# Kernel tuning notes

Hardware: AMD Instinct MI355X
Metric: run time of the kernel (lower is better)

## Reference

```python
import jax, jax.numpy as jnp
import numpy as np

VOCAB, D, BLOCK = 32000, 1024, 2048
B, S = 4, 2048

def setup_inputs() -> dict:
    key = jax.random.key(0)
    ks = jax.random.split(key, 12)
    s = 0.02
    return {
        "x": jax.random.randint(ks[0], (B, S), 0, VOCAB),
        "tok_emb": jax.random.normal(ks[1], (VOCAB, D), jnp.float32) * s,
        "pos_emb": jax.random.normal(ks[2], (BLOCK, D), jnp.float32) * s,
        "Wq": jax.random.normal(ks[3], (D, D), jnp.float32) * s,
        "bq": jnp.zeros((D,), jnp.float32),
        "Wk": jax.random.normal(ks[4], (D, D), jnp.float32) * s,
        "bk": jnp.zeros((D,), jnp.float32),
        "Wv": jax.random.normal(ks[5], (D, D), jnp.float32) * s,
        "bv": jnp.zeros((D,), jnp.float32),
        "Wfc": jax.random.normal(ks[6], (VOCAB, D), jnp.float32) * s,
        "bfc": jnp.zeros((VOCAB,), jnp.float32),
    }

def reference(x, tok_emb, pos_emb, Wq, bq, Wk, bk, Wv, bv, Wfc, bfc):
    # embeddings: token lookup + learned positional
    h = tok_emb[x] + pos_emb[jnp.arange(x.shape[1])][None, :, :]  # [B,S,D]
    Q = h @ Wq.T + bq
    K = h @ Wk.T + bk
    V = h @ Wv.T + bv
    scale = 1.0 / jnp.sqrt(jnp.float32(Q.shape[-1]))
    scores = jnp.einsum('bqd,bkd->bqk', Q, K) * scale  # [B,S,S]
    attn = jax.nn.softmax(scores, axis=-1)
    out = jnp.einsum('bqk,bkd->bqd', attn, V)
    return out @ Wfc.T + bfc  # [B,S,VOCAB]
```

## Files before the change

### kernel.cpp

```cpp
#include <hip/hip_runtime.h>
#include <hip/hip_bf16.h>
#include <stdint.h>

typedef __bf16 bf16x8 __attribute__((ext_vector_type(8)));
typedef float f32x4 __attribute__((ext_vector_type(4)));
typedef unsigned short u16x8 __attribute__((ext_vector_type(8)));

#define DEVINL static __device__ __forceinline__

DEVINL unsigned short f2bf(float f) {
  unsigned u = __builtin_bit_cast(unsigned, f);
  unsigned r = (u + 0x7FFFu + ((u >> 16) & 1u)) >> 16;
  return (unsigned short)r;
}
DEVINL float bf2f(unsigned short u) {
  return __builtin_bit_cast(float, ((unsigned)u) << 16);
}

DEVINL void gload_lds16(const unsigned short* g, unsigned short* l) {
  __builtin_amdgcn_global_load_lds(
      (const __attribute__((address_space(1))) void*)g,
      (__attribute__((address_space(3))) void*)l, 16, 0, 0);
}

__global__ __launch_bounds__(256) void embed_cvtq_kernel(
    const int* __restrict__ x, const float* __restrict__ tok,
    const float* __restrict__ pos, unsigned short* __restrict__ hb,
    const float* __restrict__ wq, const float* __restrict__ wk,
    const float* __restrict__ wv, unsigned short* __restrict__ wqkvb)
{
  if (blockIdx.x >= 8192) {
    const int b = blockIdx.x - 8192;
    for (long i = (long)b * 256 + threadIdx.x; i < 786432; i += 512 * 256) {
      const float* src;
      long off;
      if (i < 262144)      { src = wq; off = i; }
      else if (i < 524288) { src = wk; off = i - 262144; }
      else                 { src = wv; off = i - 524288; }
      float4 v = ((const float4*)src)[off];
      ushort4 o;
      o.x = f2bf(v.x); o.y = f2bf(v.y); o.z = f2bf(v.z); o.w = f2bf(v.w);
      ((ushort4*)wqkvb)[i] = o;
    }
    return;
  }
  const int bs = blockIdx.x;
  const int s  = bs & 2047;
  const long trow = (long)x[bs] * 1024;
  const int d = threadIdx.x * 4;
  const float4 t = *(const float4*)(tok + trow + d);
  const float4 p = *(const float4*)(pos + (long)s * 1024 + d);
  ushort4 o;
  o.x = f2bf(t.x + p.x);
  o.y = f2bf(t.y + p.y);
  o.z = f2bf(t.z + p.z);
  o.w = f2bf(t.w + p.w);
  *(ushort4*)(hb + (long)bs * 1024 + d) = o;
}

template<int OUTMODE>
__global__ __launch_bounds__(256) void gemm_bt(
    const unsigned short* __restrict__ A, const unsigned short* __restrict__ B,
    void* __restrict__ Cout, const float* __restrict__ bias,
    float scale, int M, int N, int K,
    long sA, long sB, long sC, int Mb, long tStride, int mapMode)
{
  __shared__ __align__(16) unsigned short lA[128 * 32];
  __shared__ __align__(16) unsigned short lB[128 * 32];
  const int tid = threadIdx.x, wid = tid >> 6, lane = tid & 63;
  int bx, by, bz;
  if (mapMode == 0) {
    bx = blockIdx.x; by = blockIdx.y; bz = blockIdx.z;
  } else {
    const int bid = blockIdx.x;
    const int g = bid & 7, jj = bid >> 3;
    bz = g >> 1;
    by = (g & 1) * 8 + (jj & 7);
    bx = jj >> 3;
  }
  A += (long)bz * sA;
  B += (long)bz * sB;
  const int bm = by * 128, bn = bx * 128;

  const int c0 = wid * 64 + lane, c1 = c0 + 256;
  const unsigned short* gA0 = A + (long)(bm + (c0 >> 2)) * K + (c0 & 3) * 8;
  const unsigned short* gA1 = A + (long)(bm + (c1 >> 2)) * K + (c1 & 3) * 8;
  const unsigned short* gB0 = B + (long)(bn + (c0 >> 2)) * K + (c0 & 3) * 8;
  const unsigned short* gB1 = B + (long)(bn + (c1 >> 2)) * K + (c1 & 3) * 8;
  unsigned short* lA0 = lA + wid * 512;
  unsigned short* lA1 = lA + 2048 + wid * 512;
  unsigned short* lB0 = lB + wid * 512;
  unsigned short* lB1 = lB + 2048 + wid * 512;

  const int wr = (wid >> 1) * 64, wc = (wid & 1) * 64;
  const int lr = lane & 15, lk = (lane >> 4) * 8;

  f32x4 acc[4][4] = {};
  const int nk = K >> 5;
  for (int kt = 0; kt < nk; ++kt) {
    const int ko = kt << 5;
    gload_lds16(gA0 + ko, lA0);
    gload_lds16(gA1 + ko, lA1);
    gload_lds16(gB0 + ko, lB0);
    gload_lds16(gB1 + ko, lB1);
    __syncthreads();
    bf16x8 af[4], bg[4];
#pragma unroll
    for (int m = 0; m < 4; ++m)
      af[m] = *(const bf16x8*)(const void*)(lA + (wr + m * 16 + lr) * 32 + lk);
#pragma unroll
    for (int n = 0; n < 4; ++n)
      bg[n] = *(const bf16x8*)(const void*)(lB + (wc + n * 16 + lr) * 32 + lk);
#pragma unroll
    for (int m = 0; m < 4; ++m)
#pragma unroll
      for (int n = 0; n < 4; ++n)
        acc[m][n] = __builtin_amdgcn_mfma_f32_16x16x32_bf16(af[m], bg[n],
                                                            acc[m][n], 0, 0, 0);
    __syncthreads();
  }

  const int r0 = bm + wr + ((lane >> 4) << 2);
  const int cbase = bn + wc + lr;
#pragma unroll
  for (int n = 0; n < 4; ++n) {
    const int col = cbase + n * 16;
    const float bv = bias ? bias[col] : 0.f;
#pragma unroll
    for (int m = 0; m < 4; ++m) {
      const int row0 = r0 + m * 16;
      if (OUTMODE == 2) {
        float* C = (float*)Cout + (long)bz * sC;
#pragma unroll
        for (int i = 0; i < 4; ++i)
          C[(long)(row0 + i) * N + col] = acc[m][n][i] * scale + bv;
      } else if (OUTMODE == 0) {
        unsigned short* C = (unsigned short*)Cout + (long)bz * sC;
#pragma unroll
        for (int i = 0; i < 4; ++i)
          C[(long)(row0 + i) * N + col] = f2bf(acc[m][n][i] * scale + bv);
      } else {
        unsigned short* C = (unsigned short*)Cout;
        const int b = row0 / Mb;
        const int srow = row0 - b * Mb;
        ushort4 o;
        o.x = f2bf(acc[m][n][0] * scale + bv);
        o.y = f2bf(acc[m][n][1] * scale + bv);
        o.z = f2bf(acc[m][n][2] * scale + bv);
        o.w = f2bf(acc[m][n][3] * scale + bv);
        *(ushort4*)(C + (long)b * tStride + (long)col * Mb + srow) = o;
      }
    }
  }
}

__global__ __launch_bounds__(256) void scores_cvt_kernel(
    const unsigned short* __restrict__ Qb, const unsigned short* __restrict__ Kb,
    unsigned short* __restrict__ Sc,
    const float* __restrict__ wfc, unsigned short* __restrict__ wfcb)
{
  __shared__ __align__(16) unsigned short lA[128 * 32];
  __shared__ __align__(16) unsigned short lB[128 * 32];
  if (blockIdx.x < 1024) {
    for (long i = (long)blockIdx.x * 256 + threadIdx.x; i < 8192000;
         i += 1024 * 256) {
      float4 v = ((const float4*)wfc)[i];
      ushort4 o;
      o.x = f2bf(v.x); o.y = f2bf(v.y); o.z = f2bf(v.z); o.w = f2bf(v.w);
      ((ushort4*)wfcb)[i] = o;
    }
    return;
  }
  constexpr int K = 1024, N = 2048;
  const int tid = threadIdx.x, wid = tid >> 6, lane = tid & 63;
  const int bid = blockIdx.x - 1024;
  const int g = bid & 7, jj = bid >> 3;
  const int bz = g >> 1;
  const int by = (g & 1) * 8 + (jj & 7);
  const int bx = jj >> 3;
  const unsigned short* A = Qb + (long)bz * (2048L * 1024);
  const unsigned short* B = Kb + (long)bz * (2048L * 1024);
  unsigned short* C = Sc + (long)bz * (2048L * 2048);
  const int bm = by * 128, bn = bx * 128;

  const int c0 = wid * 64 + lane, c1 = c0 + 256;
  const unsigned short* gA0 = A + (long)(bm + (c0 >> 2)) * K + (c0 & 3) * 8;
  const unsigned short* gA1 = A + (long)(bm + (c1 >> 2)) * K + (c1 & 3) * 8;
  const unsigned short* gB0 = B + (long)(bn + (c0 >> 2)) * K + (c0 & 3) * 8;
  const unsigned short* gB1 = B + (long)(bn + (c1 >> 2)) * K + (c1 & 3) * 8;
  unsigned short* lA0 = lA + wid * 512;
  unsigned short* lA1 = lA + 2048 + wid * 512;
  unsigned short* lB0 = lB + wid * 512;
  unsigned short* lB1 = lB + 2048 + wid * 512;

  const int wr = (wid >> 1) * 64, wc = (wid & 1) * 64;
  const int lr = lane & 15, lk = (lane >> 4) * 8;

  f32x4 acc[4][4] = {};
  for (int kt = 0; kt < 32; ++kt) {
    const int ko = kt << 5;
    gload_lds16(gA0 + ko, lA0);
    gload_lds16(gA1 + ko, lA1);
    gload_lds16(gB0 + ko, lB0);
    gload_lds16(gB1 + ko, lB1);
    __syncthreads();
    bf16x8 af[4], bg[4];
#pragma unroll
    for (int m = 0; m < 4; ++m)
      af[m] = *(const bf16x8*)(const void*)(lA + (wr + m * 16 + lr) * 32 + lk);
#pragma unroll
    for (int n = 0; n < 4; ++n)
      bg[n] = *(const bf16x8*)(const void*)(lB + (wc + n * 16 + lr) * 32 + lk);
#pragma unroll
    for (int m = 0; m < 4; ++m)
#pragma unroll
      for (int n = 0; n < 4; ++n)
        acc[m][n] = __builtin_amdgcn_mfma_f32_16x16x32_bf16(af[m], bg[n],
                                                            acc[m][n], 0, 0, 0);
    __syncthreads();
  }

  const int r0 = bm + wr + ((lane >> 4) << 2);
  const int cbase = bn + wc + lr;
#pragma unroll
  for (int n = 0; n < 4; ++n) {
    const int col = cbase + n * 16;
#pragma unroll
    for (int m = 0; m < 4; ++m) {
      const int row0 = r0 + m * 16;
#pragma unroll
      for (int i = 0; i < 4; ++i)
        C[(long)(row0 + i) * N + col] = f2bf(acc[m][n][i] * 0.03125f);
    }
  }
}

__global__ __launch_bounds__(256) void softmax_kernel(unsigned short* __restrict__ S)
{
  unsigned short* row = S + (long)blockIdx.x * 2048;
  const int t = threadIdx.x, lane = t & 63, wid = t >> 6;
  __shared__ float redm[4], reds[4];
  u16x8 raw = ((const u16x8*)row)[t];
  float v[8];
#pragma unroll
  for (int j = 0; j < 8; ++j) v[j] = bf2f(raw[j]);
  float mx = v[0];
#pragma unroll
  for (int j = 1; j < 8; ++j) mx = fmaxf(mx, v[j]);
#pragma unroll
  for (int off = 32; off; off >>= 1) mx = fmaxf(mx, __shfl_xor(mx, off, 64));
  if (lane == 0) redm[wid] = mx;
  __syncthreads();
  mx = fmaxf(fmaxf(redm[0], redm[1]), fmaxf(redm[2], redm[3]));
  float s = 0.f;
#pragma unroll
  for (int j = 0; j < 8; ++j) { v[j] = __expf(v[j] - mx); s += v[j]; }
#pragma unroll
  for (int off = 32; off; off >>= 1) s += __shfl_xor(s, off, 64);
  if (lane == 0) reds[wid] = s;
  __syncthreads();
  s = reds[0] + reds[1] + reds[2] + reds[3];
  const float inv = 1.f / s;
  u16x8 o;
#pragma unroll
  for (int j = 0; j < 8; ++j) o[j] = f2bf(v[j] * inv);
  ((u16x8*)row)[t] = o;
}

DEVINL bf16x8 ldfrag(const unsigned short* p, int row, int kx) {
  return *(const bf16x8*)((const char*)p + row * 128 + kx);
}

#define BARSB() do { __builtin_amdgcn_s_barrier(); \
                     __builtin_amdgcn_sched_barrier(0); } while (0)
#define LGK0() asm volatile("s_waitcnt lgkmcnt(0)")
#define VM6()  asm volatile("s_waitcnt vmcnt(6)")

#define MF16(rb, aArr, bArr) do { \
  _Pragma("unroll") for (int m_ = 0; m_ < 4; ++m_) \
  _Pragma("unroll") for (int n_ = 0; n_ < 4; ++n_) \
    acc[(rb) + m_][n_] = __builtin_amdgcn_mfma_f32_16x16x32_bf16( \
        aArr[m_], bArr[n_], acc[(rb) + m_][n_], 0, 0, 0); \
} while (0)

#define STG_A(b, h, gk) do { \
  const char* s_ = srcA + (h) * 262144 + (long)(((gk) & 15)) * 128; \
  gload_lds16((const unsigned short*)(s_ + la0), \
              dA + (b) * 16384 + (h) * 8192 + dO0); \
  gload_lds16((const unsigned short*)(s_ + la1), \
              dA + (b) * 16384 + (h) * 8192 + dO1); } while (0)
#define STG_B(b, h, gk) do { \
  int t_ = (gk) >> 4; if (t_ >= len) t_ = len - 1; \
  const char* s_ = Bbase + ((long)(bnStart + t_) << 19) + \
                   (h) * 262144 + (long)(((gk) & 15)) * 128; \
  gload_lds16((const unsigned short*)(s_ + la0), \
              dB + (b) * 16384 + (h) * 8192 + dO0); \
  gload_lds16((const unsigned short*)(s_ + la1), \
              dB + (b) * 16384 + (h) * 8192 + dO1); } while (0)

#define KTILE(BUF, S1, S2, S3, S4) do { \
  bf16x8 b0_[4], b1_[4], aA_[4], aB_[4], aC_[4], aD_[4]; \
  _Pragma("unroll") for (int n = 0; n < 4; ++n) { \
    b0_[n] = ldfrag(dB + (BUF) * 16384, wn * 64 + n * 16 + lr, kx0); \
    b1_[n] = ldfrag(dB + (BUF) * 16384, wn * 64 + n * 16 + lr, kx1); } \
  _Pragma("unroll") for (int m = 0; m < 4; ++m) \
    aA_[m] = ldfrag(dA + (BUF) * 16384, wm * 128 + m * 16 + lr, kx0); \
  S1; \
  BARSB(); LGK0(); __builtin_amdgcn_s_setprio(1); \
  MF16(0, aA_, b0_); \
  __builtin_amdgcn_s_setprio(0); BARSB(); \
  _Pragma("unroll") for (int m = 0; m < 4; ++m) { \
    aB_[m] = ldfrag(dA + (BUF) * 16384, wm * 128 + (4 + m) * 16 + lr, kx0); \
    aC_[m] = ldfrag(dA + (BUF) * 16384, wm * 128 + (4 + m) * 16 + lr, kx1); } \
  S2; \
  BARSB(); LGK0(); __builtin_amdgcn_s_setprio(1); \
  MF16(4, aB_, b0_); \
  __builtin_amdgcn_s_setprio(0); BARSB(); \
  _Pragma("unroll") for (int m = 0; m < 4; ++m) \
    aD_[m] = ldfrag(dA + (BUF) * 16384, wm * 128 + m * 16 + lr, kx1); \
  S3; \
  BARSB(); LGK0(); __builtin_amdgcn_s_setprio(1); \
  MF16(4, aC_, b1_); \
  __builtin_amdgcn_s_setprio(0); BARSB(); \
  S4; VM6(); \
  BARSB(); LGK0(); __builtin_amdgcn_s_setprio(1); \
  MF16(0, aD_, b1_); \
  __builtin_amdgcn_s_setprio(0); BARSB(); \
} while (0)

#define G256_PRELUDE() \
  const int tid = threadIdx.x, wid = tid >> 6, lane = tid & 63; \
  const int wm = wid >> 2, wn = wid & 3; \
  const int lr = lane & 15; \
  const int kq = (lane >> 4) << 4; \
  const int xr = (lane & 7) << 4; \
  const int kx0 = kq ^ xr; \
  const int kx1 = (64 | kq) ^ xr; \
  const int loff0 = wid * 1024 + lane * 16; \
  const int loff1 = loff0 + 8192; \
  const int r0 = loff0 >> 7, r1 = loff1 >> 7; \
  const int c0 = (loff0 & 127) ^ ((r0 & 7) << 4); \
  const int c1 = (loff1 & 127) ^ ((r1 & 7) << 4); \
  const long la0 = (long)r0 * 2048 + c0; \
  const long la1 = (long)r1 * 2048 + c1; \
  unsigned short* dA = lds; \
  unsigned short* dB = lds + 32768; \
  const int dO0 = wid * 512, dO1 = 4096 + wid * 512

__global__ __launch_bounds__(512, 2) void gemm256_fc(
    const unsigned short* __restrict__ A, const unsigned short* __restrict__ B,
    float* __restrict__ C, const float* __restrict__ bias)
{
  constexpr int N = 32000;
  __shared__ __align__(16) unsigned short lds[65536];
  G256_PRELUDE();

  const int bid = blockIdx.x;
  const int g = bid & 7;
  const int j = bid >> 3;
  const int bm = g * 4 + (j & 3);
  const int q = j >> 2;
  const int bnStart = (q < 5) ? 16 * q : 80 + (q - 5) * 15;
  const int len = (q < 5) ? 16 : 15;

  const char* srcA = (const char*)A + ((long)bm << 19);
  const char* Bbase = (const char*)B;

  f32x4 acc[8][4] = {};
  float bv[4];
#pragma unroll
  for (int n = 0; n < 4; ++n)
    bv[n] = bias[(long)bnStart * 256 + wn * 64 + n * 16 + lr];

  STG_B(0, 0, 0); STG_B(0, 1, 0); STG_A(0, 0, 0); STG_A(0, 1, 0);
  STG_B(1, 0, 1); STG_B(1, 1, 1); STG_A(1, 0, 1);
  VM6();
  BARSB();

  for (int t = 0; t < len; ++t) {
#pragma unroll 1
    for (int it = 0; it < 8; ++it) {
      const int gk = t * 16 + 2 * it;
      KTILE(0, STG_A(1, 1, gk + 1), STG_B(0, 0, gk + 2), STG_B(0, 1, gk + 2),
            STG_A(0, 0, gk + 2));
      KTILE(1, STG_A(0, 1, gk + 2), STG_B(1, 0, gk + 3), STG_B(1, 1, gk + 3),
            STG_A(1, 0, gk + 3));
    }
    const long bnRow = ((long)bnStart + t) * 256;
    const int q4 = (lane >> 4) * 4;
#pragma unroll
    for (int m = 0; m < 8; ++m) {
      const long row = (long)bm * 256 + wm * 128 + m * 16 + q4;
#pragma unroll
      for (int i = 0; i < 4; ++i) {
        float* orow = C + (row + i) * (long)N;
#pragma unroll
        for (int n = 0; n < 4; ++n)
          __builtin_nontemporal_store(acc[m][n][i] + bv[n],
                                      &orow[bnRow + wn * 64 + n * 16 + lr]);
      }
    }
    VM6();
    const int tn = (t + 1 < len) ? t + 1 : t;
#pragma unroll
    for (int n = 0; n < 4; ++n)
      bv[n] = bias[((long)bnStart + tn) * 256 + wn * 64 + n * 16 + lr];
#pragma unroll
    for (int m = 0; m < 8; ++m)
#pragma unroll
      for (int n = 0; n < 4; ++n)
        acc[m][n] = f32x4{0.f, 0.f, 0.f, 0.f};
  }
}

__global__ __launch_bounds__(512, 2) void gemm256_qkv(
    const unsigned short* __restrict__ A, const unsigned short* __restrict__ B,
    unsigned short* __restrict__ Qb, unsigned short* __restrict__ Kb,
    unsigned short* __restrict__ Vt,
    const float* __restrict__ bq, const float* __restrict__ bk,
    const float* __restrict__ bv)
{
  __shared__ __align__(16) unsigned short lds[65536];
  G256_PRELUDE();

  const int bid = blockIdx.x;
  const int g = bid & 7;
  const int j = bid >> 3;
  const int bm = g * 4 + (j & 3);
  const int q = j >> 2;
  const int bnStart = (q < 4) ? 2 * q : 8 + (q - 4);
  const int len = (q < 4) ? 2 : 1;

  const char* srcA = (const char*)A + ((long)bm << 19);
  const char* Bbase = (const char*)B;

  f32x4 acc[8][4] = {};

  STG_B(0, 0, 0); STG_B(0, 1, 0); STG_A(0, 0, 0); STG_A(0, 1, 0);
  STG_B(1, 0, 1); STG_B(1, 1, 1); STG_A(1, 0, 1);
  VM6();
  BARSB();

  for (int t = 0; t < len; ++t) {
#pragma unroll 1
    for (int it = 0; it < 8; ++it) {
      const int gk = t * 16 + 2 * it;
      KTILE(0, STG_A(1, 1, gk + 1), STG_B(0, 0, gk + 2), STG_B(0, 1, gk + 2),
            STG_A(0, 0, gk + 2));
      KTILE(1, STG_A(0, 1, gk + 2), STG_B(1, 0, gk + 3), STG_B(1, 1, gk + 3),
            STG_A(1, 0, gk + 3));
    }
    const int bnT = bnStart + t;
    const int sector = bnT >> 2;
    const int colb = (bnT & 3) * 256;
    const float* bias_s = (sector == 0) ? bq : (sector == 1) ? bk : bv;
    const int q4 = (lane >> 4) * 4;
    if (sector < 2) {
      unsigned short* C = (sector == 0) ? Qb : Kb;
#pragma unroll
      for (int n = 0; n < 4; ++n) {
        const int col = colb + wn * 64 + n * 16 + lr;
        const float bb = bias_s[col];
#pragma unroll
        for (int m = 0; m < 8; ++m) {
          const long row = (long)bm * 256 + wm * 128 + m * 16 + q4;
#pragma unroll
          for (int i = 0; i < 4; ++i)
            C[(row + i) * 1024 + col] = f2bf(acc[m][n][i] + bb);
        }
      }
    } else {
#pragma unroll
      for (int n = 0; n < 4; ++n) {
        const int col = colb + wn * 64 + n * 16 + lr;
        const float bb = bias_s[col];
#pragma unroll
        for (int m = 0; m < 8; ++m) {
          const long row = (long)bm * 256 + wm * 128 + m * 16 + q4;
          const int b = (int)(row >> 11);
          const int srow = (int)(row & 2047);
          ushort4 o;
          o.x = f2bf(acc[m][n][0] + bb);
          o.y = f2bf(acc[m][n][1] + bb);
          o.z = f2bf(acc[m][n][2] + bb);
          o.w = f2bf(acc[m][n][3] + bb);
          *(ushort4*)(Vt + (long)b * (1024L * 2048) + (long)col * 2048 + srow) = o;
        }
      }
    }
    VM6();
#pragma unroll
    for (int m = 0; m < 8; ++m)
#pragma unroll
      for (int n = 0; n < 4; ++n)
        acc[m][n] = f32x4{0.f, 0.f, 0.f, 0.f};
  }
}

extern "C" void kernel_launch(void* const* d_in, const int* in_sizes, int n_in,
                              void* d_out, int out_size, void* d_ws, size_t ws_size,
                              hipStream_t stream)
{
  const int*   x   = (const int*)d_in[0];
  const float* tok = (const float*)d_in[1];
  const float* pos = (const float*)d_in[2];
  const float* Wq  = (const float*)d_in[3];
  const float* bq  = (const float*)d_in[4];
  const float* Wk  = (const float*)d_in[5];
  const float* bk  = (const float*)d_in[6];
  const float* Wv  = (const float*)d_in[7];
  const float* bv  = (const float*)d_in[8];
  const float* Wfc = (const float*)d_in[9];
  const float* bfc = (const float*)d_in[10];
  float* out = (float*)d_out;

  char* ws = (char*)d_ws;
  unsigned short* hb   = (unsigned short*)(ws);
  unsigned short* Wqb  = (unsigned short*)(ws + 16777216);
  unsigned short* Wfcb = (unsigned short*)(ws + 23068672);
  unsigned short* Qb   = (unsigned short*)(ws + 88604672);
  unsigned short* Kb   = (unsigned short*)(ws + 105381888);
  unsigned short* Vt   = (unsigned short*)(ws + 122159104);
  unsigned short* Sc   = (unsigned short*)(ws + 138936320);
  unsigned short* AO   = hb;

  dim3 blk(256);
  embed_cvtq_kernel<<<dim3(8704), blk, 0, stream>>>(x, tok, pos, hb,
                                                    Wq, Wk, Wv, Wqb);
  gemm256_qkv<<<dim3(256), dim3(512), 0, stream>>>(hb, Wqb, Qb, Kb, Vt,
                                                   bq, bk, bv);
  scores_cvt_kernel<<<dim3(2048), blk, 0, stream>>>(Qb, Kb, Sc, Wfc, Wfcb);
  softmax_kernel<<<8192, 256, 0, stream>>>(Sc);
  gemm_bt<0><<<dim3(512), blk, 0, stream>>>(Sc, Vt, AO, nullptr, 1.f,
      2048, 1024, 2048, 2048L * 2048, 1024L * 2048, 2048L * 1024, 0, 0, 1);
  gemm256_fc<<<dim3(256), dim3(512), 0, stream>>>(AO, Wfcb, out, bfc);
}
```

Baseline: 749.5 us.

## Replace 256x256 FC GEMM with 128x256 tile, triple-buffered LDS pipeline

Swaps the output projection GEMM from 256x256 tiles with 2 blocks per CU to 128x256 tiles over 512 blocks, with launch bounds asking for 4 waves per SIMD. The new kernel uses a three-stage LDS ring with k-step 32, loads via global_load_lds with an XOR swizzle, and gives the MFMA section higher priority. The aim is better occupancy and load balance across CUs, and more latency hiding on the largest GEMM. In exchange, A/B reuse per block is lower and global traffic for Wfc roughly doubles.

```diff
diff --git a/kernel.cpp b/kernel.cpp
--- a/kernel.cpp
+++ b/kernel.cpp
@@ -347,72 +347,6 @@
   unsigned short* dB = lds + 32768; \
   const int dO0 = wid * 512, dO1 = 4096 + wid * 512
 
-__global__ __launch_bounds__(512, 2) void gemm256_fc(
-    const unsigned short* __restrict__ A, const unsigned short* __restrict__ B,
-    float* __restrict__ C, const float* __restrict__ bias)
-{
-  constexpr int N = 32000;
-  __shared__ __align__(16) unsigned short lds[65536];
-  G256_PRELUDE();
-
-  const int bid = blockIdx.x;
-  const int g = bid & 7;
-  const int j = bid >> 3;
-  const int bm = g * 4 + (j & 3);
-  const int q = j >> 2;
-  const int bnStart = (q < 5) ? 16 * q : 80 + (q - 5) * 15;
-  const int len = (q < 5) ? 16 : 15;
-
-  const char* srcA = (const char*)A + ((long)bm << 19);
-  const char* Bbase = (const char*)B;
-
-  f32x4 acc[8][4] = {};
-  float bv[4];
-#pragma unroll
-  for (int n = 0; n < 4; ++n)
-    bv[n] = bias[(long)bnStart * 256 + wn * 64 + n * 16 + lr];
-
-  STG_B(0, 0, 0); STG_B(0, 1, 0); STG_A(0, 0, 0); STG_A(0, 1, 0);
-  STG_B(1, 0, 1); STG_B(1, 1, 1); STG_A(1, 0, 1);
-  VM6();
-  BARSB();
-
-  for (int t = 0; t < len; ++t) {
-#pragma unroll 1
-    for (int it = 0; it < 8; ++it) {
-      const int gk = t * 16 + 2 * it;
-      KTILE(0, STG_A(1, 1, gk + 1), STG_B(0, 0, gk + 2), STG_B(0, 1, gk + 2),
-            STG_A(0, 0, gk + 2));
-      KTILE(1, STG_A(0, 1, gk + 2), STG_B(1, 0, gk + 3), STG_B(1, 1, gk + 3),
-            STG_A(1, 0, gk + 3));
-    }
-    const long bnRow = ((long)bnStart + t) * 256;
-    const int q4 = (lane >> 4) * 4;
-#pragma unroll
-    for (int m = 0; m < 8; ++m) {
-      const long row = (long)bm * 256 + wm * 128 + m * 16 + q4;
-#pragma unroll
-      for (int i = 0; i < 4; ++i) {
-        float* orow = C + (row + i) * (long)N;
-#pragma unroll
-        for (int n = 0; n < 4; ++n)
-          __builtin_nontemporal_store(acc[m][n][i] + bv[n],
-                                      &orow[bnRow + wn * 64 + n * 16 + lr]);
-      }
-    }
-    VM6();
-    const int tn = (t + 1 < len) ? t + 1 : t;
-#pragma unroll
-    for (int n = 0; n < 4; ++n)
-      bv[n] = bias[((long)bnStart + tn) * 256 + wn * 64 + n * 16 + lr];
-#pragma unroll
-    for (int m = 0; m < 8; ++m)
-#pragma unroll
-      for (int n = 0; n < 4; ++n)
-        acc[m][n] = f32x4{0.f, 0.f, 0.f, 0.f};
-  }
-}
-
 __global__ __launch_bounds__(512, 2) void gemm256_qkv(
     const unsigned short* __restrict__ A, const unsigned short* __restrict__ B,
     unsigned short* __restrict__ Qb, unsigned short* __restrict__ Kb,
@@ -497,6 +431,130 @@
   }
 }
 
+__global__ __launch_bounds__(512, 4) void gemm128_fc(
+    const unsigned short* __restrict__ A, const unsigned short* __restrict__ B,
+    float* __restrict__ C, const float* __restrict__ bias)
+{
+  constexpr int N = 32000;
+  __shared__ __align__(16) char lds[3 * 24576];
+  const int tid = threadIdx.x, wid = tid >> 6, lane = tid & 63;
+  const int wm = wid >> 2, wn = wid & 3;
+  const int lr = lane & 15, q = lane >> 4;
+
+  const int bid = blockIdx.x;
+  const int g = bid & 7;
+  const int j = bid >> 3;
+  const int bm = g * 8 + (j & 7);
+  const int q8 = j >> 3;
+  const int bnStart = (q8 < 5) ? 16 * q8 : 80 + (q8 - 5) * 15;
+  const int len = (q8 < 5) ? 16 : 15;
+  const int lastK = len * 32 - 1;
+
+  const int o = tid * 16;
+  const int rA = o >> 6, pA = (o >> 4) & 3;
+  const int fA = (rA ^ (rA >> 2)) & 3;
+  const long sA_off = (long)rA * 2048 + ((pA ^ fA) << 4);
+  const int rB1 = rA, rB2 = rA + 128;
+  const int fB1 = fA;
+  const int fB2 = (rB2 ^ (rB2 >> 2)) & 3;
+  const long sB1_off = (long)rB1 * 2048 + ((pA ^ fB1) << 4);
+  const long sB2_off = (long)rB2 * 2048 + ((pA ^ fB2) << 4);
+  const char* srcA = (const char*)A + ((long)bm << 18);
+  const char* Bbase = (const char*)B;
+
+  int aoff[4], boff[4];
+#pragma unroll
+  for (int m = 0; m < 4; ++m) {
+    const int r = wm * 64 + m * 16 + lr;
+    aoff[m] = r * 64 + ((q ^ ((r ^ (r >> 2)) & 3)) << 4);
+  }
+#pragma unroll
+  for (int n = 0; n < 4; ++n) {
+    const int r = wn * 64 + n * 16 + lr;
+    boff[n] = r * 64 + ((q ^ ((r ^ (r >> 2)) & 3)) << 4);
+  }
+
+  f32x4 acc[4][4] = {};
+  float bv[4];
+#pragma unroll
+  for (int n = 0; n < 4; ++n)
+    bv[n] = bias[(long)bnStart * 256 + wn * 64 + n * 16 + lr];
+
+#define STG3_FC(kk, buf) do { \
+    const int kc = (kk) <= lastK ? (kk) : lastK; \
+    int tt = kc >> 5; \
+    const long kb = (long)(kc & 31) * 64; \
+    char* db = lds + (buf) * 24576; \
+    gload_lds16((const unsigned short*)(srcA + kb + sA_off), \
+                (unsigned short*)(db + o)); \
+    const char* sB = Bbase + ((long)(bnStart + tt) << 19) + kb; \
+    gload_lds16((const unsigned short*)(sB + sB1_off), \
+                (unsigned short*)(db + 8192 + o)); \
+    gload_lds16((const unsigned short*)(sB + sB2_off), \
+                (unsigned short*)(db + 16384 + o)); \
+  } while (0)
+
+  STG3_FC(0, 0);
+  STG3_FC(1, 1);
+
+  int cur = 0, nxt = 1, pre = 2;
+  for (int t = 0; t < len; ++t) {
+#pragma unroll 1
+    for (int ks = 0; ks < 32; ++ks) {
+      const int gk = t * 32 + ks;
+      STG3_FC(gk + 2, pre);
+      asm volatile("s_waitcnt vmcnt(6)");
+      __builtin_amdgcn_s_barrier();
+      __builtin_amdgcn_sched_barrier(0);
+      const char* pAb = lds + cur * 24576;
+      const char* pBb = pAb + 8192;
+      bf16x8 af[4], bg[4];
+#pragma unroll
+      for (int m = 0; m < 4; ++m)
+        af[m] = *(const bf16x8*)(pAb + aoff[m]);
+#pragma unroll
+      for (int n = 0; n < 4; ++n)
+        bg[n] = *(const bf16x8*)(pBb + boff[n]);
+      __builtin_amdgcn_s_setprio(1);
+#pragma unroll
+      for (int m = 0; m < 4; ++m)
+#pragma unroll
+        for (int n = 0; n < 4; ++n)
+          acc[m][n] = __builtin_amdgcn_mfma_f32_16x16x32_bf16(af[m], bg[n],
+                                                              acc[m][n], 0, 0, 0);
+      __builtin_amdgcn_s_setprio(0);
+      __builtin_amdgcn_s_barrier();
+      __builtin_amdgcn_sched_barrier(0);
+      const int tmp = cur; cur = nxt; nxt = pre; pre = tmp;
+    }
+    const long bnRow = ((long)bnStart + t) * 256;
+    const int q4 = q * 4;
+#pragma unroll
+    for (int m = 0; m < 4; ++m) {
+      const long row = (long)bm * 128 + wm * 64 + m * 16 + q4;
+#pragma unroll
+      for (int i = 0; i < 4; ++i) {
+        float* orow = C + (row + i) * (long)N;
+#pragma unroll
+        for (int n = 0; n < 4; ++n)
+          __builtin_nontemporal_store(acc[m][n][i] + bv[n],
+                                      &orow[bnRow + wn * 64 + n * 16 + lr]);
+      }
+    }
+    asm volatile("s_waitcnt vmcnt(6)");
+    const int tn = (t + 1 < len) ? t + 1 : t;
+#pragma unroll
+    for (int n = 0; n < 4; ++n)
+      bv[n] = bias[((long)bnStart + tn) * 256 + wn * 64 + n * 16 + lr];
+#pragma unroll
+    for (int m = 0; m < 4; ++m)
+#pragma unroll
+      for (int n = 0; n < 4; ++n)
+        acc[m][n] = f32x4{0.f, 0.f, 0.f, 0.f};
+  }
+#undef STG3_FC
+}
+
 extern "C" void kernel_launch(void* const* d_in, const int* in_sizes, int n_in,
                               void* d_out, int out_size, void* d_ws, size_t ws_size,
                               hipStream_t stream)
@@ -533,5 +591,5 @@
   softmax_kernel<<<8192, 256, 0, stream>>>(Sc);
   gemm_bt<0><<<dim3(512), blk, 0, stream>>>(Sc, Vt, AO, nullptr, 1.f,
       2048, 1024, 2048, 2048L * 2048, 1024L * 2048, 2048L * 1024, 0, 0, 1);
-  gemm256_fc<<<dim3(256), dim3(512), 0, stream>>>(AO, Wfcb, out, bfc);
-}
+  gemm128_fc<<<dim3(512), dim3(512), 0, stream>>>(AO, Wfcb, out, bfc);
+}
```

Result: slower. 834.6 us (+11.4%).
